# Performance work log

Measured on AMD Instinct MI355X. Metric: run time of the kernel, lower is better.

The kernel has to match this reference:

```python
import jax, jax.numpy as jnp
import numpy as np

B, S, D = 1, 1024, 1024
NH, DH, DR = 8, 128, 64
DCQ, DC = 768, 256
INTER, E, TOPK = 512, 8, 2

def rmsnorm(x, w, eps=1e-6):
    return x * jax.lax.rsqrt(jnp.mean(x * x, -1, keepdims=True) + eps) * w

def lin(x, w, b):
    return x @ w.T + b

def apply_rope(x, cos, sin):
    # x: [b, s, h, d]; cos/sin: [S, d//2]; complex rotate pairs (even, odd)
    b, s, h, d = x.shape
    xr = x.reshape(b, s, h, d // 2, 2)
    x0, x1 = xr[..., 0], xr[..., 1]
    c = cos[None, :s, None, :]
    sn = sin[None, :s, None, :]
    return jnp.stack([x0 * c - x1 * sn, x0 * sn + x1 * c], -1).reshape(b, s, h, d)

def setup_inputs():
    keys = iter(jax.random.split(jax.random.key(0), 64))
    def nrm(*shape):
        return jax.random.normal(next(keys), shape, jnp.float32) * 0.02
    theta = 1.0 / (10000.0 ** (jnp.arange(0, DR, 2, dtype=jnp.float32) / DR))
    ang = jnp.arange(S, dtype=jnp.float32)[:, None] * theta[None, :]
    return dict(
        h=jax.random.normal(next(keys), (B, S, D), jnp.float32),
        freqs_cos=jnp.cos(ang), freqs_sin=jnp.sin(ang),
        mask=jnp.triu(jnp.ones((S, S), bool), 1),
        attn_norm_w=jnp.ones(D), ffn_norm_w=jnp.ones(D),
        wq_down=nrm(DCQ, D), bq_down=jnp.zeros(DCQ), q_norm_w=jnp.ones(DCQ),
        wqc=nrm(NH * DH, DCQ), bqc=jnp.zeros(NH * DH),
        wqr=nrm(NH * DR, DCQ), bqr=jnp.zeros(NH * DR),
        wkr=nrm(DR, D), bkr=jnp.zeros(DR), kr_norm_w=jnp.ones(DR),
        wkv_down=nrm(DC, D), bkv_down=jnp.zeros(DC), kv_norm_w=jnp.ones(DC),
        wkc=nrm(NH * DH, DC), bkc=jnp.zeros(NH * DH),
        wvc=nrm(NH * DH, DC), bvc=jnp.zeros(NH * DH),
        wo=nrm(D, NH * DH), bo=jnp.zeros(D),
        sw1=nrm(INTER, D), sb1=jnp.zeros(INTER), sw2=nrm(D, INTER), sb2=jnp.zeros(D),
        sw3=nrm(INTER, D), sb3=jnp.zeros(INTER),
        ew1=nrm(E, INTER, D), eb1=jnp.zeros((E, INTER)), ew2=nrm(E, D, INTER), eb2=jnp.zeros((E, D)),
        ew3=nrm(E, INTER, D), eb3=jnp.zeros((E, INTER)),
        centroids=jax.random.normal(next(keys), (E, D), jnp.float32), biases=jnp.zeros(E),
    )

def _forward(h, freqs_cos, freqs_sin, mask, attn_norm_w, ffn_norm_w, wq_down, bq_down, q_norm_w, wqc, bqc, wqr, bqr, wkr, bkr, kr_norm_w, wkv_down, bkv_down, kv_norm_w, wkc, bkc, wvc, bvc, wo, bo, sw1, sb1, sw2, sb2, sw3, sb3, ew1, eb1, ew2, eb2, ew3, eb3, centroids, biases):
    b, s, _ = h.shape
    # --- pre-norm MLA attention ---
    x = rmsnorm(h, attn_norm_w)
    cQ = rmsnorm(lin(x, wq_down, bq_down), q_norm_w)
    qR = apply_rope(lin(cQ, wqr, bqr).reshape(b, s, NH, DR), freqs_cos, freqs_sin)
    qC = lin(cQ, wqc, bqc).reshape(b, s, NH, DH)
    q = jnp.concatenate([qC, qR], -1)                      # [b,s,NH,DH+DR]
    kR = apply_rope(rmsnorm(lin(x, wkr, bkr), kr_norm_w).reshape(b, s, 1, DR), freqs_cos, freqs_sin)
    cKV = rmsnorm(lin(x, wkv_down, bkv_down), kv_norm_w)
    kC = lin(cKV, wkc, bkc).reshape(b, s, NH, DH)
    vC = lin(cKV, wvc, bvc).reshape(b, s, NH, DH)
    k = jnp.concatenate([jnp.broadcast_to(kR, (b, s, NH, DR)), kC], -1)  # source order: [kR, kC]
    scores = jnp.einsum('bqhd,bkhd->bhqk', q, k) / jnp.sqrt(jnp.float32(DH + DR))
    scores = jnp.where(mask[None, None], jnp.finfo(scores.dtype).min, scores)
    attw = jax.nn.softmax(scores, -1)                      # dropout in eval mode = identity
    attn = jnp.einsum('bhqk,bkhd->bqhd', attw, vC).reshape(b, s, NH * DH)
    x1 = h + lin(attn, wo, bo)
    # --- pre-norm MoE FFN ---
    y = rmsnorm(x1, ffn_norm_w)
    shared = lin(jax.nn.silu(lin(y, sw1, sb1)) * lin(y, sw3, sb3), sw2, sb2)  # mean over 1 shared expert
    affinity = jax.nn.sigmoid(y @ centroids.T)             # [b,s,E]
    _, topi = jax.lax.top_k(affinity + biases, TOPK)
    gates = jax.nn.softmax(jnp.take_along_axis(affinity, topi, -1), -1)      # [b,s,TOPK]
    combine = (jax.nn.one_hot(topi, E, dtype=y.dtype) * gates[..., None]).sum(-2)  # [b,s,E]
    h1 = jax.nn.silu(jnp.einsum('bsd,eid->bsei', y, ew1) + eb1) * (jnp.einsum('bsd,eid->bsei', y, ew3) + eb3)
    out_e = jnp.einsum('bsei,edi->bsed', h1, ew2) + eb2
    routed = (out_e * combine[..., None]).sum(2)
    return x1 + shared + routed

def reference(h, freqs_cos, freqs_sin, mask, attn_norm_w, ffn_norm_w, wq_down, bq_down, q_norm_w, wqc, bqc, wqr, bqr, wkr, bkr, kr_norm_w, wkv_down, bkv_down, kv_norm_w, wkc, bkc, wvc, bvc, wo, bo, sw1, sb1, sw2, sb2, sw3, sb3, ew1, eb1, ew2, eb2, ew3, eb3, centroids, biases):
    return _forward(h, freqs_cos, freqs_sin, mask, attn_norm_w, ffn_norm_w, wq_down, bq_down, q_norm_w, wqc, bqc, wqr, bqr, wkr, bkr, kr_norm_w, wkv_down, bkv_down, kv_norm_w, wkc, bkc, wvc, bvc, wo, bo, sw1, sb1, sw2, sb2, sw3, sb3, ew1, eb1, ew2, eb2, ew3, eb3, centroids, biases)
```

## Files before the change

kernel.cpp:

```cpp
#include <hip/hip_runtime.h>

typedef unsigned short u16;
typedef __attribute__((ext_vector_type(8))) short short8;
typedef __attribute__((ext_vector_type(4))) float f32x4;

__device__ __forceinline__ float b2f(u16 u) { return __uint_as_float(((unsigned)u) << 16); }
__device__ __forceinline__ u16 f2b(float f) {
    unsigned x = __float_as_uint(f);
    return (u16)((x + 0x7fffu + ((x >> 16) & 1u)) >> 16);
}

#define GLDS16(gp, lp) __builtin_amdgcn_global_load_lds( \
    (const __attribute__((address_space(1))) void*)(gp), \
    (__attribute__((address_space(3))) void*)(lp), 16, 0, 0)

#define WAITV(N) do { \
    asm volatile("s_waitcnt vmcnt(" #N ")" ::: "memory"); \
    __builtin_amdgcn_sched_barrier(0); \
} while (0)

#define KC8_SWZ(lane) ((((lane) & 3) ^ (((lane) >> 3) & 3)) << 3)
#define RD_SWZ(fm, fq) (((fq) ^ (((fm) >> 1) & 3)) << 3)

struct Seg { const u16* W; const float* bias; void* C; int ldc; int epi; int bx0; int aidx; };
struct GArgs {
    const u16* A[2]; int lda[2]; int K[2];
    Seg seg[4]; int nseg;
    const float* res;
    float* dst2;
};

__launch_bounds__(256)
__global__ void mgemm4(GArgs ga)
{
    __shared__ u16 As[6 * 2048];
    __shared__ u16 Bs[6 * 2048];
    int bx = blockIdx.x, by = blockIdx.y;
    int si = 0;
#pragma unroll
    for (int i = 1; i < 4; i++)
        if (i < ga.nseg && bx >= ga.seg[i].bx0) si = i;
    const u16* Wp = ga.seg[si].W;
    const float* bp = ga.seg[si].bias;
    void* Cp = ga.seg[si].C;
    const int ldco = ga.seg[si].ldc;
    const int epi = ga.seg[si].epi;
    const int ai = ga.seg[si].aidx;
    const u16* Ap = ga.A[ai];
    const int lda = ga.lda[ai], K = ga.K[ai];
    const int col0 = (bx - ga.seg[si].bx0) * 64;
    const int row0 = by * 64;

    int tid = threadIdx.x;
    int lane = tid & 63, w = tid >> 6;
    int r0 = (w << 4) + (lane >> 2), kc8 = KC8_SWZ(lane);
    const u16* gA = Ap + (size_t)(row0 + r0) * lda + kc8;
    const u16* gB = Wp + (size_t)(col0 + r0) * lda + kc8;

    int fm = lane & 15, fq = lane >> 4;
    const int so = RD_SWZ(fm, fq);
    f32x4 acc[4] = {};

#define MG_STAGE(BS, KO) do { \
    GLDS16(gA + (KO), As + (BS) * 2048 + (w << 9)); \
    GLDS16(gB + (KO), Bs + (BS) * 2048 + (w << 9)); \
} while (0)

    const int nst = K >> 5;
    MG_STAGE(0, 0); MG_STAGE(1, 32); MG_STAGE(2, 64); MG_STAGE(3, 96);
    int bcur = 0;
    for (int t = 0; t < nst; t += 2) {
        if (t < nst - 2) { WAITV(4); } else { WAITV(0); }
        __builtin_amdgcn_s_barrier();
        int w4 = bcur + 4; if (w4 >= 6) w4 -= 6;
        int w5 = w4 + 1;   if (w5 >= 6) w5 -= 6;
        if (t + 4 < nst) MG_STAGE(w4, (t + 4) << 5);
        if (t + 5 < nst) MG_STAGE(w5, (t + 5) << 5);
#pragma unroll
        for (int sub = 0; sub < 2; sub++) {
            int bc = bcur + sub; if (bc >= 6) bc -= 6;
            short8 af = *(const short8*)(As + bc * 2048 + (w << 9) + fm * 32 + so);
            short8 bf[4];
#pragma unroll
            for (int nt = 0; nt < 4; nt++)
                bf[nt] = *(const short8*)(Bs + bc * 2048 + ((nt << 4) + fm) * 32 + so);
#pragma unroll
            for (int nt = 0; nt < 4; nt++)
                acc[nt] = __builtin_amdgcn_mfma_f32_16x16x32_bf16(af, bf[nt], acc[nt], 0, 0, 0);
        }
        bcur += 2; if (bcur >= 6) bcur -= 6;
    }
#undef MG_STAGE

    int rbase = row0 + (w << 4) + (fq << 2);
#pragma unroll
    for (int nt = 0; nt < 4; nt++) {
        int c = col0 + (nt << 4) + fm;
        float bcol = bp[c];
#pragma unroll
        for (int reg = 0; reg < 4; reg++) {
            int r = rbase + reg;
            float v = acc[nt][reg] + bcol;
            if (epi == 3)
                ((u16*)Cp)[(size_t)r * ldco + c] = f2b(v);
            else if (epi == 1) {
                float o = v + ga.res[(size_t)r * ldco + c];
                ((float*)Cp)[(size_t)r * ldco + c] = o;
                if (ga.dst2) ga.dst2[(size_t)r * ldco + c] = o;
            } else
                ((float*)Cp)[(size_t)r * ldco + c] = v;
        }
    }
}

__launch_bounds__(256)
__global__ void mega_glu(const u16* __restrict__ Y16,
                         const u16* __restrict__ sw1, const float* __restrict__ sb1,
                         const u16* __restrict__ sw3, const float* __restrict__ sb3,
                         const u16* __restrict__ ew1, const float* __restrict__ eb1,
                         const u16* __restrict__ ew3, const float* __restrict__ eb3,
                         u16* __restrict__ Gb,
                         const int* __restrict__ lists, const int* __restrict__ counts)
{
    __shared__ u16 As[6 * 2048];
    __shared__ u16 B1s[6 * 2048];
    __shared__ u16 B3s[6 * 2048];
    int bx = blockIdx.x, by = blockIdx.y, z = blockIdx.z;
    int col0 = bx * 64;
    int cnt = 1024; const int* list = nullptr;
    const u16 *W1p, *W3p; const float *b1p, *b3p;
    if (z == 0) {
        W1p = sw1; b1p = sb1; W3p = sw3; b3p = sb3;
    } else {
        int e = z - 1; cnt = counts[e]; list = lists + (e << 10);
        W1p = ew1 + (size_t)e * 512 * 1024; b1p = eb1 + e * 512;
        W3p = ew3 + (size_t)e * 512 * 1024; b3p = eb3 + e * 512;
    }
    int row0 = by * 64;
    if (row0 >= cnt) return;
    u16* Cp = Gb + (size_t)z * 524288;

    int tid = threadIdx.x, lane = tid & 63, w = tid >> 6;
    int r0 = (w << 4) + (lane >> 2), kc8 = KC8_SWZ(lane);
    int ar = row0 + r0;
    if (z > 0) ar = list[ar < cnt ? ar : cnt - 1];
    const u16* gA = Y16 + (size_t)ar * 1024 + kc8;
    const u16* gB1 = W1p + (size_t)(col0 + r0) * 1024 + kc8;
    const u16* gB3 = W3p + (size_t)(col0 + r0) * 1024 + kc8;

    int fm = lane & 15, fq = lane >> 4;
    const int so = RD_SWZ(fm, fq);
    f32x4 accU[4] = {}, accV[4] = {};

#define GL_STAGE(BS, KO) do { \
    GLDS16(gA + (KO),  As  + (BS) * 2048 + (w << 9)); \
    GLDS16(gB1 + (KO), B1s + (BS) * 2048 + (w << 9)); \
    GLDS16(gB3 + (KO), B3s + (BS) * 2048 + (w << 9)); \
} while (0)

    GL_STAGE(0, 0); GL_STAGE(1, 32); GL_STAGE(2, 64); GL_STAGE(3, 96);
    int bcur = 0;
    for (int t = 0; t < 32; t += 2) {
        if (t < 30) { WAITV(6); } else { WAITV(0); }
        __builtin_amdgcn_s_barrier();
        int w4 = bcur + 4; if (w4 >= 6) w4 -= 6;
        int w5 = w4 + 1;   if (w5 >= 6) w5 -= 6;
        if (t + 4 < 32) GL_STAGE(w4, (t + 4) << 5);
        if (t + 5 < 32) GL_STAGE(w5, (t + 5) << 5);
#pragma unroll
        for (int sub = 0; sub < 2; sub++) {
            int bc = bcur + sub; if (bc >= 6) bc -= 6;
            short8 af = *(const short8*)(As + bc * 2048 + (w << 9) + fm * 32 + so);
#pragma unroll
            for (int nt = 0; nt < 4; nt++) {
                short8 b1 = *(const short8*)(B1s + bc * 2048 + ((nt << 4) + fm) * 32 + so);
                accU[nt] = __builtin_amdgcn_mfma_f32_16x16x32_bf16(af, b1, accU[nt], 0, 0, 0);
            }
#pragma unroll
            for (int nt = 0; nt < 4; nt++) {
                short8 b3 = *(const short8*)(B3s + bc * 2048 + ((nt << 4) + fm) * 32 + so);
                accV[nt] = __builtin_amdgcn_mfma_f32_16x16x32_bf16(af, b3, accV[nt], 0, 0, 0);
            }
        }
        bcur += 2; if (bcur >= 6) bcur -= 6;
    }
#undef GL_STAGE

    int rbase = row0 + (w << 4) + (fq << 2);
#pragma unroll
    for (int nt = 0; nt < 4; nt++) {
        int c = col0 + (nt << 4) + fm;
        float b1c = b1p[c], b3c = b3p[c];
#pragma unroll
        for (int reg = 0; reg < 4; reg++) {
            int r = rbase + reg;
            if (r >= cnt) continue;
            float u = b2f(f2b(accU[nt][reg] + b1c));
            float v = b2f(f2b(accV[nt][reg] + b3c));
            Cp[(size_t)r * 512 + c] = f2b(u / (1.f + __expf(-u)) * v);
        }
    }
}

__launch_bounds__(256)
__global__ void mega_down(const u16* __restrict__ Gb,
                          const u16* __restrict__ sw2, const float* __restrict__ sb2,
                          const u16* __restrict__ ew2, const float* __restrict__ eb2,
                          float* __restrict__ out,
                          const int* __restrict__ lists, const float* __restrict__ glist,
                          const int* __restrict__ counts)
{
    __shared__ u16 Gs[6 * 2048];
    __shared__ u16 Ws[6 * 2048];
    int bx = blockIdx.x, by = blockIdx.y, z = blockIdx.z;
    int cnt = 1024; const int* list = nullptr; const float* gl = nullptr;
    const u16* Wp; const float* bp;
    if (z == 0) { Wp = sw2; bp = sb2; }
    else {
        int e = z - 1;
        cnt = counts[e]; list = lists + (e << 10); gl = glist + (e << 10);
        Wp = ew2 + (size_t)e * 1024 * 512; bp = eb2 + e * 1024;
    }
    int row0 = by * 64;
    if (row0 >= cnt) return;
    const u16* Ap = Gb + (size_t)z * 524288;
    int col0 = bx * 64;

    int tid = threadIdx.x, lane = tid & 63, w = tid >> 6;
    int r0 = (w << 4) + (lane >> 2), kc8 = KC8_SWZ(lane);
    const u16* gG = Ap + (size_t)(row0 + r0) * 512 + kc8;
    const u16* gW = Wp + (size_t)(col0 + r0) * 512 + kc8;

    int fm = lane & 15, fq = lane >> 4;
    const int so = RD_SWZ(fm, fq);
    f32x4 acc[4] = {};

#define MD_STAGE(BS, KO) do { \
    GLDS16(gG + (KO), Gs + (BS) * 2048 + (w << 9)); \
    GLDS16(gW + (KO), Ws + (BS) * 2048 + (w << 9)); \
} while (0)

    MD_STAGE(0, 0); MD_STAGE(1, 32); MD_STAGE(2, 64); MD_STAGE(3, 96);
    int bcur = 0;
    for (int t = 0; t < 16; t += 2) {
        if (t < 14) { WAITV(4); } else { WAITV(0); }
        __builtin_amdgcn_s_barrier();
        int w4 = bcur + 4; if (w4 >= 6) w4 -= 6;
        int w5 = w4 + 1;   if (w5 >= 6) w5 -= 6;
        if (t + 4 < 16) MD_STAGE(w4, (t + 4) << 5);
        if (t + 5 < 16) MD_STAGE(w5, (t + 5) << 5);
#pragma unroll
        for (int sub = 0; sub < 2; sub++) {
            int bc = bcur + sub; if (bc >= 6) bc -= 6;
            short8 af = *(const short8*)(Gs + bc * 2048 + (w << 9) + fm * 32 + so);
            short8 bf[4];
#pragma unroll
            for (int nt = 0; nt < 4; nt++)
                bf[nt] = *(const short8*)(Ws + bc * 2048 + ((nt << 4) + fm) * 32 + so);
#pragma unroll
            for (int nt = 0; nt < 4; nt++)
                acc[nt] = __builtin_amdgcn_mfma_f32_16x16x32_bf16(af, bf[nt], acc[nt], 0, 0, 0);
        }
        bcur += 2; if (bcur >= 6) bcur -= 6;
    }
#undef MD_STAGE

    int rbase = row0 + (w << 4) + (fq << 2);
#pragma unroll
    for (int nt = 0; nt < 4; nt++) {
        int c = col0 + (nt << 4) + fm;
        float bcol = bp[c];
#pragma unroll
        for (int reg = 0; reg < 4; reg++) {
            int r = rbase + reg;
            int tok; float g;
            if (z == 0) { tok = r; g = 1.f; }
            else { if (r >= cnt) continue; tok = list[r]; g = gl[r]; }
            atomicAdd(&out[(size_t)tok * 1024 + c], g * (acc[nt][reg] + bcol));
        }
    }
}

__launch_bounds__(256)
__global__ void attn_mfma(const u16* __restrict__ Qp, const u16* __restrict__ Kp,
                          const u16* __restrict__ VT,
                          float* __restrict__ Opart, float* __restrict__ MLp)
{
    const int qt = blockIdx.x, h = blockIdx.y, z = blockIdx.z;
    const int q0 = qt * 64;
    const int tid = threadIdx.x;
    const int lane = tid & 63, w = tid >> 6;
    const int fm = lane & 15, fq = lane >> 4;

    __shared__ u16 Ks[2 * 12288];
    __shared__ u16 Vs[4 * 4096];
    __shared__ u16 Ps[4 * 2048];

    const u16* qrow = Qp + ((size_t)h * 1024 + q0 + w * 16 + fm) * 192;
    short8 qf[6];
#pragma unroll
    for (int c = 0; c < 6; c++)
        qf[c] = *(const short8*)(qrow + c * 32 + fq * 8);

    const u16* Kb = Kp + (size_t)h * 1024 * 192;
    const u16* Vb = VT + (size_t)h * 128 * 1024;

    float m_i[4], l_i[4];
#pragma unroll
    for (int r = 0; r < 4; r++) { m_i[r] = -1e30f; l_i[r] = 0.f; }
    f32x4 accO[8] = {};
    const float scale = 0.07216878364870323f;
    const int nkt = (qt >> 1) + 1;
    const int half0 = (nkt + 1) >> 1;
    const int ktlo = z ? half0 : 0;
    const int kthi = z ? nkt : half0;
    const int rbase = w * 16 + fq * 4;

    for (int kt = ktlo; kt < kthi; ++kt) {
        const int kt0 = kt * 128;
#pragma unroll
        for (int half = 0; half < 2; half++) {
            const int o = kt0 + half * 64;
#pragma unroll
            for (int i = 0; i < 6; i++) {
                int idx = w + 4 * i;
                int c = idx >> 2, k4 = idx & 3;
                const u16* g = Kb + (size_t)(o + k4 * 16 + (lane >> 2)) * 192 + c * 32 + (lane & 3) * 8;
                GLDS16(g, Ks + half * 12288 + c * 2048 + k4 * 512 + lane * 8);
            }
#pragma unroll
            for (int i = 0; i < 4; i++) {
                int idx = w + 4 * i;
                int kc = idx >> 3, k8 = idx & 7;
                const u16* g = Vb + (size_t)(k8 * 16 + (lane >> 2)) * 1024 + o + kc * 32 + (lane & 3) * 8;
                GLDS16(g, Vs + (half * 2 + kc) * 4096 + k8 * 512 + lane * 8);
            }
        }
        __syncthreads();
        f32x4 sacc[8];
        __builtin_amdgcn_s_setprio(1);
#pragma unroll
        for (int nt = 0; nt < 8; nt++) {
            sacc[nt] = (f32x4){0.f, 0.f, 0.f, 0.f};
#pragma unroll
            for (int c = 0; c < 6; c++) {
                short8 kf = *(const short8*)(Ks + (nt >> 2) * 12288 + c * 2048 + ((nt & 3) * 16 + fm) * 32 + fq * 8);
                sacc[nt] = __builtin_amdgcn_mfma_f32_16x16x32_bf16(qf[c], kf, sacc[nt], 0, 0, 0);
            }
        }
        __builtin_amdgcn_s_setprio(0);
        float pv[8][4], rmax[4];
#pragma unroll
        for (int reg = 0; reg < 4; reg++) {
            int q = q0 + rbase + reg;
            float mx = -1e30f;
#pragma unroll
            for (int nt = 0; nt < 8; nt++) {
                int gk = kt0 + nt * 16 + fm;
                float s = sacc[nt][reg] * scale;
                if (gk > q) s = -1e30f;
                pv[nt][reg] = s;
                mx = fmaxf(mx, s);
            }
            rmax[reg] = mx;
        }
#pragma unroll
        for (int m = 1; m < 16; m <<= 1)
#pragma unroll
            for (int reg = 0; reg < 4; reg++)
                rmax[reg] = fmaxf(rmax[reg], __shfl_xor(rmax[reg], m));
        float alpha[4], rsum[4];
#pragma unroll
        for (int reg = 0; reg < 4; reg++) {
            float mn = fmaxf(m_i[reg], rmax[reg]);
            alpha[reg] = __expf(m_i[reg] - mn);
            m_i[reg] = mn;
            float s = 0.f;
#pragma unroll
            for (int nt = 0; nt < 8; nt++) {
                float p = __expf(pv[nt][reg] - mn);
                pv[nt][reg] = p;
                s += p;
            }
            rsum[reg] = s;
        }
#pragma unroll
        for (int m = 1; m < 16; m <<= 1)
#pragma unroll
            for (int reg = 0; reg < 4; reg++)
                rsum[reg] += __shfl_xor(rsum[reg], m);
#pragma unroll
        for (int reg = 0; reg < 4; reg++)
            l_i[reg] = l_i[reg] * alpha[reg] + rsum[reg];
#pragma unroll
        for (int nt = 0; nt < 8; nt++)
#pragma unroll
            for (int reg = 0; reg < 4; reg++)
                Ps[w * 2048 + (nt >> 1) * 512 + (fq * 4 + reg) * 32 + (nt & 1) * 16 + fm]
                    = f2b(pv[nt][reg]);
#pragma unroll
        for (int n2 = 0; n2 < 8; n2++)
#pragma unroll
            for (int reg = 0; reg < 4; reg++)
                accO[n2][reg] *= alpha[reg];
        short8 pf[4];
#pragma unroll
        for (int kc = 0; kc < 4; kc++)
            pf[kc] = *(const short8*)(Ps + w * 2048 + kc * 512 + fm * 32 + fq * 8);
        __builtin_amdgcn_s_setprio(1);
#pragma unroll
        for (int n2 = 0; n2 < 8; n2++)
#pragma unroll
            for (int kc = 0; kc < 4; kc++) {
                short8 vf = *(const short8*)(Vs + kc * 4096 + (n2 * 16 + fm) * 32 + fq * 8);
                accO[n2] = __builtin_amdgcn_mfma_f32_16x16x32_bf16(pf[kc], vf, accO[n2], 0, 0, 0);
            }
        __builtin_amdgcn_s_setprio(0);
        __syncthreads();
    }
    float* Ob = Opart + ((size_t)(z * 8 + h) * 1024) * 128;
#pragma unroll
    for (int reg = 0; reg < 4; reg++) {
        int row = q0 + rbase + reg;
#pragma unroll
        for (int n2 = 0; n2 < 8; n2++)
            Ob[(size_t)row * 128 + n2 * 16 + fm] = accO[n2][reg];
        if (fm == 0) {
            MLp[((size_t)(z * 8 + h) * 1024 + row) * 2]     = m_i[reg];
            MLp[((size_t)(z * 8 + h) * 1024 + row) * 2 + 1] = l_i[reg];
        }
    }
}

__launch_bounds__(256)
__global__ void attn_combine(const float* __restrict__ Opart,
                             const float* __restrict__ MLp,
                             u16* __restrict__ O)
{
    int tid = threadIdx.x;
    int rowg = blockIdx.x * 16 + (tid >> 4);
    int h = rowg >> 10, row = rowg & 1023;
    int c0 = (tid & 15) * 8;
    const float* O0 = Opart + ((size_t)h * 1024 + row) * 128;
    const float* O1 = Opart + ((size_t)(8 + h) * 1024 + row) * 128;
    float m0 = MLp[((size_t)h * 1024 + row) * 2];
    float l0 = MLp[((size_t)h * 1024 + row) * 2 + 1];
    float m1 = MLp[((size_t)(8 + h) * 1024 + row) * 2];
    float l1 = MLp[((size_t)(8 + h) * 1024 + row) * 2 + 1];
    float M = fmaxf(m0, m1);
    float w0 = __expf(m0 - M), w1 = __expf(m1 - M);
    float inv = 1.f / (l0 * w0 + l1 * w1);
#pragma unroll
    for (int j = 0; j < 8; j++) {
        float o = (O0[c0 + j] * w0 + O1[c0 + j] * w1) * inv;
        O[(size_t)row * 1024 + h * 128 + c0 + j] = f2b(o);
    }
}

__launch_bounds__(256)
__global__ void rmsnorm2x(const float* __restrict__ X0, const float* __restrict__ w0,
                          u16* __restrict__ O0, int c0,
                          const float* __restrict__ X1, const float* __restrict__ w1,
                          u16* __restrict__ O1, int c1)
{
    int b = blockIdx.x, tid = threadIdx.x;
    const float* X; const float* w; u16* O; int cols; int r;
    if (b < 1024) { X = X0; w = w0; O = O0; cols = c0; r = b; }
    else          { X = X1; w = w1; O = O1; cols = c1; r = b - 1024; }
    const float* xr = X + (size_t)r * cols;
    float ss = 0.f;
    for (int j = tid; j < cols; j += 256) { float v = xr[j]; ss += v * v; }
    __shared__ float red[256];
    red[tid] = ss; __syncthreads();
    for (int st = 128; st > 0; st >>= 1) { if (tid < st) red[tid] += red[tid + st]; __syncthreads(); }
    float scale = rsqrtf(red[0] / cols + 1e-6f);
    for (int j = tid; j < cols; j += 256)
        O[(size_t)r * cols + j] = f2b(xr[j] * scale * w[j]);
}

__launch_bounds__(256)
__global__ void rmsnorm_route(const float* __restrict__ X1, const float* __restrict__ ffnw,
                              u16* __restrict__ Y16,
                              const float* __restrict__ cent, const float* __restrict__ biases,
                              int* __restrict__ counts, int* __restrict__ lists,
                              float* __restrict__ glist)
{
    __shared__ float red[256];
    int b = blockIdx.x, tid = threadIdx.x;
    if (b < 1024) {
        int r = b;
        const float* xr = X1 + (size_t)r * 1024;
        float ss = 0.f;
        for (int j = tid; j < 1024; j += 256) { float v = xr[j]; ss += v * v; }
        red[tid] = ss; __syncthreads();
        for (int st = 128; st > 0; st >>= 1) { if (tid < st) red[tid] += red[tid + st]; __syncthreads(); }
        float scale = rsqrtf(red[0] / 1024.f + 1e-6f);
        for (int j = tid; j < 1024; j += 256)
            Y16[(size_t)r * 1024 + j] = f2b(xr[j] * scale * ffnw[j]);
    } else {
        int t = b - 1024;
        const float* xr = X1 + (size_t)t * 1024;
        float ss = 0.f;
        float acc[8] = {};
        for (int j = tid; j < 1024; j += 256) {
            float x = xr[j];
            ss += x * x;
            float yp = x * ffnw[j];
#pragma unroll
            for (int e = 0; e < 8; e++) acc[e] += yp * cent[e * 1024 + j];
        }
        red[tid] = ss; __syncthreads();
        for (int st = 128; st > 0; st >>= 1) { if (tid < st) red[tid] += red[tid + st]; __syncthreads(); }
        float scale = rsqrtf(red[0] / 1024.f + 1e-6f);
        __syncthreads();
        __shared__ float aff[8];
        for (int e = 0; e < 8; e++) {
            red[tid] = acc[e]; __syncthreads();
            for (int st = 128; st > 0; st >>= 1) { if (tid < st) red[tid] += red[tid + st]; __syncthreads(); }
            if (tid == 0) aff[e] = 1.f / (1.f + expf(-red[0] * scale));
            __syncthreads();
        }
        if (tid == 0) {
            float sb[8];
#pragma unroll
            for (int e = 0; e < 8; e++) sb[e] = aff[e] + biases[e];
            int i0 = 0;
            for (int e = 1; e < 8; e++) if (sb[e] > sb[i0]) i0 = e;
            int i1 = -1;
            for (int e = 0; e < 8; e++) { if (e == i0) continue; if (i1 < 0 || sb[e] > sb[i1]) i1 = e; }
            float a0 = aff[i0], a1 = aff[i1];
            float mx = fmaxf(a0, a1);
            float e0 = expf(a0 - mx), e1 = expf(a1 - mx);
            float inv = 1.f / (e0 + e1);
            int p0 = atomicAdd(&counts[i0], 1);
            lists[i0 * 1024 + p0] = t; glist[i0 * 1024 + p0] = e0 * inv;
            int p1 = atomicAdd(&counts[i1], 1);
            lists[i1 * 1024 + p1] = t; glist[i1 * 1024 + p1] = e1 * inv;
        }
    }
}

__launch_bounds__(256)
__global__ void pack_all(const float* __restrict__ QC, const float* __restrict__ QRr,
                         const float* __restrict__ KRraw, const float* __restrict__ krw,
                         const float* __restrict__ KC,
                         const u16* __restrict__ VCb,
                         const float* __restrict__ fcos, const float* __restrict__ fsin,
                         u16* __restrict__ Qp, u16* __restrict__ Kp, u16* __restrict__ VT)
{
    __shared__ u16 Ts[64][68];
    __shared__ float kshared[64];
    int b = blockIdx.x, tid = threadIdx.x;
    if (b < 1024) {
        int s = b;
        if (tid < 64) {
            float v = KRraw[(size_t)s * 64 + tid];
            float ss = v * v;
#pragma unroll
            for (int m = 1; m < 64; m <<= 1) ss += __shfl_xor(ss, m);
            float scale = rsqrtf(ss / 64.f + 1e-6f);
            int j = tid >> 1;
            float c = fcos[s * 32 + j], sn = fsin[s * 32 + j];
            float x0 = KRraw[(size_t)s * 64 + (tid & ~1)] * scale * krw[tid & ~1];
            float x1 = KRraw[(size_t)s * 64 + (tid | 1)]  * scale * krw[tid | 1];
            kshared[tid] = (tid & 1) ? (x0 * sn + x1 * c) : (x0 * c - x1 * sn);
        }
        __syncthreads();
        for (int e = tid; e < 1536; e += 256) {
            int h = e / 192, d = e % 192;
            float q;
            if (d < 128) {
                q = QC[(size_t)s * 1024 + h * 128 + d];
            } else {
                int dd = d - 128, j = dd >> 1;
                float c = fcos[s * 32 + j], sn = fsin[s * 32 + j];
                float x0 = QRr[(size_t)s * 512 + h * 64 + (dd & ~1)];
                float x1 = QRr[(size_t)s * 512 + h * 64 + (dd | 1)];
                q = (dd & 1) ? (x0 * sn + x1 * c) : (x0 * c - x1 * sn);
            }
            Qp[((size_t)h * 1024 + s) * 192 + d] = f2b(q);
            float k = (d < 64) ? kshared[d]
                               : KC[(size_t)s * 1024 + h * 128 + d - 64];
            Kp[((size_t)h * 1024 + s) * 192 + d] = f2b(k);
        }
    } else {
        int idx = b - 1024;
        int s0 = (idx & 15) * 64, d0 = (idx >> 4) * 64;
        for (int k = 0; k < 16; k++) {
            int e = tid + k * 256, r = e >> 6, c = e & 63;
            Ts[r][c] = VCb[(size_t)(s0 + r) * 1024 + d0 + c];
        }
        __syncthreads();
        for (int k = 0; k < 16; k++) {
            int e = tid + k * 256, d = e >> 6, s = e & 63;
            VT[(size_t)(d0 + d) * 1024 + s0 + s] = Ts[s][d];
        }
    }
}

#define NCAST 4096
__launch_bounds__(256)
__global__ void fused_cast(const float* p0, const float* p1, const float* p2,
                           const float* p3, const float* p4, const float* p5,
                           const float* p6, const float* p7, const float* p8,
                           const float* p9, const float* p10, const float* p11,
                           const float* p12, const float* pkr,
                           u16* __restrict__ dst,
                           const float* __restrict__ hX, const float* __restrict__ attnw,
                           u16* __restrict__ X16)
{
    __shared__ float red[256];
    int b = blockIdx.x, tid = threadIdx.x;
    if (b < NCAST) {
        const int NQ = 18022400 / 4;
        for (int i = b * 256 + tid; i < NQ; i += NCAST * 256) {
            int e = i * 4;
            const float* s; int base;
            if      (e <   786432) { s = p0;  base = 0; }
            else if (e <  1048576) { s = p1;  base =   786432; }
            else if (e <  1835008) { s = p2;  base =  1048576; }
            else if (e <  2228224) { s = p3;  base =  1835008; }
            else if (e <  2490368) { s = p4;  base =  2228224; }
            else if (e <  2752512) { s = p5;  base =  2490368; }
            else if (e <  3801088) { s = p6;  base =  2752512; }
            else if (e <  4325376) { s = p7;  base =  3801088; }
            else if (e <  4849664) { s = p8;  base =  4325376; }
            else if (e <  5373952) { s = p9;  base =  4849664; }
            else if (e <  9568256) { s = p10; base =  5373952; }
            else if (e < 13762560) { s = p11; base =  9568256; }
            else if (e < 17956864) { s = p12; base = 13762560; }
            else                   { s = pkr; base = 17956864; }
            float4 v = *(const float4*)(s + (e - base));
            ushort4 o;
            o.x = f2b(v.x); o.y = f2b(v.y); o.z = f2b(v.z); o.w = f2b(v.w);
            *(ushort4*)(dst + e) = o;
        }
    } else {
        int r = b - NCAST;
        const float* xr = hX + (size_t)r * 1024;
        float ss = 0.f;
        for (int j = tid; j < 1024; j += 256) { float v = xr[j]; ss += v * v; }
        red[tid] = ss; __syncthreads();
        for (int st = 128; st > 0; st >>= 1) { if (tid < st) red[tid] += red[tid + st]; __syncthreads(); }
        float scale = rsqrtf(red[0] / 1024.f + 1e-6f);
        for (int j = tid; j < 1024; j += 256)
            X16[(size_t)r * 1024 + j] = f2b(xr[j] * scale * attnw[j]);
    }
}

extern "C" void kernel_launch(void* const* d_in, const int* in_sizes, int n_in,
                              void* d_out, int out_size, void* d_ws, size_t ws_size,
                              hipStream_t stream)
{
    (void)in_sizes; (void)n_in; (void)ws_size; (void)out_size;
    const float* h       = (const float*)d_in[0];
    const float* fcos    = (const float*)d_in[1];
    const float* fsin    = (const float*)d_in[2];
    const float* attn_w  = (const float*)d_in[4];
    const float* ffn_w   = (const float*)d_in[5];
    const float* wq_down = (const float*)d_in[6];
    const float* bq_down = (const float*)d_in[7];
    const float* q_norm  = (const float*)d_in[8];
    const float* wqc     = (const float*)d_in[9];
    const float* bqc     = (const float*)d_in[10];
    const float* wqr     = (const float*)d_in[11];
    const float* bqr     = (const float*)d_in[12];
    const float* wkr     = (const float*)d_in[13];
    const float* bkr     = (const float*)d_in[14];
    const float* kr_norm = (const float*)d_in[15];
    const float* wkv     = (const float*)d_in[16];
    const float* bkv     = (const float*)d_in[17];
    const float* kv_norm = (const float*)d_in[18];
    const float* wkc     = (const float*)d_in[19];
    const float* bkc     = (const float*)d_in[20];
    const float* wvc     = (const float*)d_in[21];
    const float* bvc     = (const float*)d_in[22];
    const float* wo      = (const float*)d_in[23];
    const float* bo      = (const float*)d_in[24];
    const float* sw1     = (const float*)d_in[25];
    const float* sb1     = (const float*)d_in[26];
    const float* sw2     = (const float*)d_in[27];
    const float* sb2     = (const float*)d_in[28];
    const float* sw3     = (const float*)d_in[29];
    const float* sb3     = (const float*)d_in[30];
    const float* ew1     = (const float*)d_in[31];
    const float* eb1     = (const float*)d_in[32];
    const float* ew2     = (const float*)d_in[33];
    const float* eb2     = (const float*)d_in[34];
    const float* ew3     = (const float*)d_in[35];
    const float* eb3     = (const float*)d_in[36];
    const float* cent    = (const float*)d_in[37];
    const float* biases  = (const float*)d_in[38];

    char* wsb = (char*)d_ws;
    const size_t U5 = 512 * 1024;
    u16*   X16   = (u16*)(wsb + 8 * U5);
    float* QRr   = (float*)(wsb + 12 * U5);
    float* CQraw = (float*)(wsb + 16 * U5);
    u16*   ATT16 = (u16*)(wsb + 16 * U5);
    u16*   CQ16  = (u16*)(wsb + 22 * U5);
    float* CKVraw= (float*)(wsb + 25 * U5);
    u16*   CKV16 = (u16*)(wsb + 27 * U5);
    float* KRraw = (float*)(wsb + 28 * U5);
    float* QC    = (float*)(wsb + 29 * U5);
    float* KC    = (float*)(wsb + 37 * U5);
    float* X1    = (float*)(wsb + 53 * U5);
    float* GL    = (float*)(wsb + 61 * U5);
    int*   lists = (int*)(wsb + 61 * U5 + 32 * 1024);
    int*   counts= (int*)(wsb + 61 * U5 + 64 * 1024);
    u16*   Y16   = (u16*)(wsb + 69 * U5);
    u16*   Gb    = (u16*)(wsb + 73 * U5);

    u16* wb = (u16*)(wsb + 92 * U5);
    u16 *c_wq  = wb;
    u16 *c_wkv = c_wq  + 786432;
    u16 *c_wqc = c_wkv + 262144;
    u16 *c_wqr = c_wqc + 786432;
    u16 *c_wkc = c_wqr + 393216;
    u16 *c_wvc = c_wkc + 262144;
    u16 *c_wo  = c_wvc + 262144;
    u16 *c_sw1 = c_wo  + 1048576;
    u16 *c_sw3 = c_sw1 + 524288;
    u16 *c_sw2 = c_sw3 + 524288;
    u16 *c_ew1 = c_sw2 + 524288;
    u16 *c_ew3 = c_ew1 + 4194304;
    u16 *c_ew2 = c_ew3 + 4194304;
    u16 *c_wkr = c_ew2 + 4194304;
    u16* VCb = (u16*)(wsb + 92 * U5 + 36175872);
    u16* VTp = VCb + 1048576;
    u16* Qpk = VTp + 1048576;
    u16* Kpk = Qpk + 1572864;
    float* Opart = (float*)(wsb + 192 * U5);
    float* MLp   = (float*)(wsb + 209 * U5);

    fused_cast<<<NCAST + 1024, 256, 0, stream>>>(wq_down, wkv, wqc, wqr, wkc, wvc, wo,
                                                 sw1, sw3, sw2, ew1, ew3, ew2, wkr, wb,
                                                 h, attn_w, X16);

    {
        GArgs g = {};
        g.A[0] = X16; g.lda[0] = 1024; g.K[0] = 1024;
        g.seg[0] = { c_wq,  bq_down, CQraw,  768, 0, 0,  0 };
        g.seg[1] = { c_wkv, bkv,     CKVraw, 256, 0, 12, 0 };
        g.seg[2] = { c_wkr, bkr,     KRraw,  64,  0, 16, 0 };
        g.nseg = 3;
        mgemm4<<<dim3(17, 16), 256, 0, stream>>>(g);
    }
    rmsnorm2x<<<2048, 256, 0, stream>>>(CQraw, q_norm, CQ16, 768,
                                        CKVraw, kv_norm, CKV16, 256);
    {
        GArgs g = {};
        g.A[0] = CQ16;  g.lda[0] = 768; g.K[0] = 768;
        g.A[1] = CKV16; g.lda[1] = 256; g.K[1] = 256;
        g.seg[0] = { c_wqc, bqc, QC,   1024, 0, 0,  0 };
        g.seg[1] = { c_wqr, bqr, QRr,  512,  0, 16, 0 };
        g.seg[2] = { c_wkc, bkc, KC,   1024, 0, 24, 1 };
        g.seg[3] = { c_wvc, bvc, VCb,  1024, 3, 40, 1 };
        g.nseg = 4;
        mgemm4<<<dim3(56, 16), 256, 0, stream>>>(g);
    }
    pack_all<<<1280, 256, 0, stream>>>(QC, QRr, KRraw, kr_norm, KC, VCb, fcos, fsin,
                                       Qpk, Kpk, VTp);
    attn_mfma<<<dim3(16, 8, 2), 256, 0, stream>>>(Qpk, Kpk, VTp, Opart, MLp);
    attn_combine<<<512, 256, 0, stream>>>(Opart, MLp, ATT16);
    {
        GArgs g = {};
        g.A[0] = ATT16; g.lda[0] = 1024; g.K[0] = 1024;
        g.seg[0] = { c_wo, bo, X1, 1024, 1, 0, 0 };
        g.nseg = 1; g.res = h; g.dst2 = (float*)d_out;
        mgemm4<<<dim3(16, 16), 256, 0, stream>>>(g);
    }

    hipMemsetAsync(counts, 0, 32, stream);
    rmsnorm_route<<<2048, 256, 0, stream>>>(X1, ffn_w, Y16, cent, biases,
                                            counts, lists, GL);
    mega_glu<<<dim3(8, 16, 9), 256, 0, stream>>>(Y16, c_sw1, sb1, c_sw3, sb3,
                                                 c_ew1, eb1, c_ew3, eb3,
                                                 Gb, lists, counts);
    mega_down<<<dim3(16, 16, 9), 256, 0, stream>>>(Gb, c_sw2, sb2, c_ew2, eb2,
                                                   (float*)d_out, lists, GL, counts);
}
```

Measured before the change: 354.8 us.

## Swizzle blocks across XCDs, fuse attention combine, replace FFN atomics with gather combine

Adds an XCD-aware block index remap to the GEMM, GLU and down kernels so neighbouring tiles share an L2. The split-K attention combine moves into attn_mfma, where the last-finishing block of each tile, detected through an atomic flag counter, does the merge. The memset of the routing counters moves into fused_cast. The down projection now writes per-expert results to a scratch buffer instead of doing atomicAdd scatter, and a new ffn_combine kernel gathers the shared and top-2 expert outputs per token. This trades atomic contention for an extra scratch write and read pass plus one more launch.

```diff
diff --git a/kernel.cpp b/kernel.cpp
--- a/kernel.cpp
+++ b/kernel.cpp
@@ -21,6 +21,15 @@
 
 #define KC8_SWZ(lane) ((((lane) & 3) ^ (((lane) >> 3) & 3)) << 3)
 #define RD_SWZ(fm, fq) (((fq) ^ (((fm) >> 1) & 3)) << 3)
+
+__device__ __forceinline__ void xcd_swz(int& bx, int& by) {
+    if ((gridDim.x & 7) == 0 && gridDim.y == 16) {
+        int lid = bx + by * gridDim.x;
+        int q = lid >> 3, r = lid & 7;
+        by = q & 15;
+        bx = r + ((q >> 4) << 3);
+    }
+}
 
 struct Seg { const u16* W; const float* bias; void* C; int ldc; int epi; int bx0; int aidx; };
 struct GArgs {
@@ -36,6 +45,7 @@
     __shared__ u16 As[6 * 2048];
     __shared__ u16 Bs[6 * 2048];
     int bx = blockIdx.x, by = blockIdx.y;
+    xcd_swz(bx, by);
     int si = 0;
 #pragma unroll
     for (int i = 1; i < 4; i++)
@@ -126,6 +136,7 @@
     __shared__ u16 B1s[6 * 2048];
     __shared__ u16 B3s[6 * 2048];
     int bx = blockIdx.x, by = blockIdx.y, z = blockIdx.z;
+    xcd_swz(bx, by);
     int col0 = bx * 64;
     int cnt = 1024; const int* list = nullptr;
     const u16 *W1p, *W3p; const float *b1p, *b3p;
@@ -206,25 +217,26 @@
 __global__ void mega_down(const u16* __restrict__ Gb,
                           const u16* __restrict__ sw2, const float* __restrict__ sb2,
                           const u16* __restrict__ ew2, const float* __restrict__ eb2,
-                          float* __restrict__ out,
-                          const int* __restrict__ lists, const float* __restrict__ glist,
+                          float* __restrict__ Dscr,
                           const int* __restrict__ counts)
 {
     __shared__ u16 Gs[6 * 2048];
     __shared__ u16 Ws[6 * 2048];
     int bx = blockIdx.x, by = blockIdx.y, z = blockIdx.z;
-    int cnt = 1024; const int* list = nullptr; const float* gl = nullptr;
+    xcd_swz(bx, by);
+    int cnt = 1024;
     const u16* Wp; const float* bp;
     if (z == 0) { Wp = sw2; bp = sb2; }
     else {
         int e = z - 1;
-        cnt = counts[e]; list = lists + (e << 10); gl = glist + (e << 10);
+        cnt = counts[e];
         Wp = ew2 + (size_t)e * 1024 * 512; bp = eb2 + e * 1024;
     }
     int row0 = by * 64;
     if (row0 >= cnt) return;
     const u16* Ap = Gb + (size_t)z * 524288;
     int col0 = bx * 64;
+    float* Dp = Dscr + (size_t)z * 1048576;
 
     int tid = threadIdx.x, lane = tid & 63, w = tid >> 6;
     int r0 = (w << 4) + (lane >> 2), kc8 = KC8_SWZ(lane);
@@ -273,18 +285,38 @@
 #pragma unroll
         for (int reg = 0; reg < 4; reg++) {
             int r = rbase + reg;
-            int tok; float g;
-            if (z == 0) { tok = r; g = 1.f; }
-            else { if (r >= cnt) continue; tok = list[r]; g = gl[r]; }
-            atomicAdd(&out[(size_t)tok * 1024 + c], g * (acc[nt][reg] + bcol));
-        }
-    }
+            Dp[(size_t)r * 1024 + c] = acc[nt][reg] + bcol;
+        }
+    }
+}
+
+__launch_bounds__(256)
+__global__ void ffn_combine(const float* __restrict__ Dscr,
+                            const int* __restrict__ sE, const int* __restrict__ sP,
+                            const float* __restrict__ sG,
+                            float* __restrict__ out)
+{
+    int t = blockIdx.x, tid = threadIdx.x;
+    int e0 = sE[t * 2], e1 = sE[t * 2 + 1];
+    int p0 = sP[t * 2], p1 = sP[t * 2 + 1];
+    float g0 = sG[t * 2], g1 = sG[t * 2 + 1];
+    const float4* Ds = (const float4*)(Dscr + (size_t)t * 1024);
+    const float4* D0 = (const float4*)(Dscr + (size_t)(e0 + 1) * 1048576 + (size_t)p0 * 1024);
+    const float4* D1 = (const float4*)(Dscr + (size_t)(e1 + 1) * 1048576 + (size_t)p1 * 1024);
+    float4* o = (float4*)(out + (size_t)t * 1024);
+    float4 a = o[tid], s = Ds[tid], x0 = D0[tid], x1 = D1[tid];
+    a.x += s.x + g0 * x0.x + g1 * x1.x;
+    a.y += s.y + g0 * x0.y + g1 * x1.y;
+    a.z += s.z + g0 * x0.z + g1 * x1.z;
+    a.w += s.w + g0 * x0.w + g1 * x1.w;
+    o[tid] = a;
 }
 
 __launch_bounds__(256)
 __global__ void attn_mfma(const u16* __restrict__ Qp, const u16* __restrict__ Kp,
                           const u16* __restrict__ VT,
-                          float* __restrict__ Opart, float* __restrict__ MLp)
+                          float* __restrict__ Opart, float* __restrict__ MLp,
+                          int* __restrict__ flags, u16* __restrict__ O16)
 {
     const int qt = blockIdx.x, h = blockIdx.y, z = blockIdx.z;
     const int q0 = qt * 64;
@@ -430,30 +462,34 @@
             MLp[((size_t)(z * 8 + h) * 1024 + row) * 2 + 1] = l_i[reg];
         }
     }
-}
-
-__launch_bounds__(256)
-__global__ void attn_combine(const float* __restrict__ Opart,
-                             const float* __restrict__ MLp,
-                             u16* __restrict__ O)
-{
-    int tid = threadIdx.x;
-    int rowg = blockIdx.x * 16 + (tid >> 4);
-    int h = rowg >> 10, row = rowg & 1023;
-    int c0 = (tid & 15) * 8;
-    const float* O0 = Opart + ((size_t)h * 1024 + row) * 128;
-    const float* O1 = Opart + ((size_t)(8 + h) * 1024 + row) * 128;
-    float m0 = MLp[((size_t)h * 1024 + row) * 2];
-    float l0 = MLp[((size_t)h * 1024 + row) * 2 + 1];
-    float m1 = MLp[((size_t)(8 + h) * 1024 + row) * 2];
-    float l1 = MLp[((size_t)(8 + h) * 1024 + row) * 2 + 1];
-    float M = fmaxf(m0, m1);
-    float w0 = __expf(m0 - M), w1 = __expf(m1 - M);
-    float inv = 1.f / (l0 * w0 + l1 * w1);
-#pragma unroll
-    for (int j = 0; j < 8; j++) {
-        float o = (O0[c0 + j] * w0 + O1[c0 + j] * w1) * inv;
-        O[(size_t)row * 1024 + h * 128 + c0 + j] = f2b(o);
+    __shared__ int oldv_s;
+    __threadfence();
+    __syncthreads();
+    if (tid == 0)
+        oldv_s = __hip_atomic_fetch_add(flags + qt * 8 + h, 1,
+                                        __ATOMIC_ACQ_REL, __HIP_MEMORY_SCOPE_AGENT);
+    __syncthreads();
+    if (oldv_s != 1) return;
+    __threadfence();
+    const float* O0 = Opart + ((size_t)h * 1024) * 128;
+    const float* O1 = Opart + ((size_t)(8 + h) * 1024) * 128;
+    for (int i = tid; i < 2048; i += 256) {
+        int row = q0 + (i >> 5);
+        int c4 = (i & 31) << 2;
+        float m0 = MLp[((size_t)h * 1024 + row) * 2];
+        float l0 = MLp[((size_t)h * 1024 + row) * 2 + 1];
+        float m1 = MLp[((size_t)(8 + h) * 1024 + row) * 2];
+        float l1 = MLp[((size_t)(8 + h) * 1024 + row) * 2 + 1];
+        float M = fmaxf(m0, m1);
+        float w0 = __expf(m0 - M), w1 = __expf(m1 - M);
+        float inv = 1.f / (l0 * w0 + l1 * w1);
+        float4 a = *(const float4*)(O0 + (size_t)row * 128 + c4);
+        float4 b = *(const float4*)(O1 + (size_t)row * 128 + c4);
+        u16* op = O16 + (size_t)row * 1024 + h * 128 + c4;
+        op[0] = f2b((a.x * w0 + b.x * w1) * inv);
+        op[1] = f2b((a.y * w0 + b.y * w1) * inv);
+        op[2] = f2b((a.z * w0 + b.z * w1) * inv);
+        op[3] = f2b((a.w * w0 + b.w * w1) * inv);
     }
 }
 
@@ -483,7 +519,8 @@
                               u16* __restrict__ Y16,
                               const float* __restrict__ cent, const float* __restrict__ biases,
                               int* __restrict__ counts, int* __restrict__ lists,
-                              float* __restrict__ glist)
+                              int* __restrict__ sE, int* __restrict__ sP,
+                              float* __restrict__ sG)
 {
     __shared__ float red[256];
     int b = blockIdx.x, tid = threadIdx.x;
@@ -533,9 +570,11 @@
             float e0 = expf(a0 - mx), e1 = expf(a1 - mx);
             float inv = 1.f / (e0 + e1);
             int p0 = atomicAdd(&counts[i0], 1);
-            lists[i0 * 1024 + p0] = t; glist[i0 * 1024 + p0] = e0 * inv;
+            lists[i0 * 1024 + p0] = t;
             int p1 = atomicAdd(&counts[i1], 1);
-            lists[i1 * 1024 + p1] = t; glist[i1 * 1024 + p1] = e1 * inv;
+            lists[i1 * 1024 + p1] = t;
+            sE[t * 2] = i0; sP[t * 2] = p0; sG[t * 2] = e0 * inv;
+            sE[t * 2 + 1] = i1; sP[t * 2 + 1] = p1; sG[t * 2 + 1] = e1 * inv;
         }
     }
 }
@@ -607,7 +646,7 @@
                            const float* p12, const float* pkr,
                            u16* __restrict__ dst,
                            const float* __restrict__ hX, const float* __restrict__ attnw,
-                           u16* __restrict__ X16)
+                           u16* __restrict__ X16, int* __restrict__ zc)
 {
     __shared__ float red[256];
     int b = blockIdx.x, tid = threadIdx.x;
@@ -637,6 +676,7 @@
         }
     } else {
         int r = b - NCAST;
+        if (r == 0 && tid < 136) zc[tid] = 0;
         const float* xr = hX + (size_t)r * 1024;
         float ss = 0.f;
         for (int j = tid; j < 1024; j += 256) { float v = xr[j]; ss += v * v; }
@@ -705,9 +745,12 @@
     float* QC    = (float*)(wsb + 29 * U5);
     float* KC    = (float*)(wsb + 37 * U5);
     float* X1    = (float*)(wsb + 53 * U5);
-    float* GL    = (float*)(wsb + 61 * U5);
+    int*   counts= (int*)(wsb + 61 * U5 + 64 * 1024);
+    int*   flags = counts + 8;
     int*   lists = (int*)(wsb + 61 * U5 + 32 * 1024);
-    int*   counts= (int*)(wsb + 61 * U5 + 64 * 1024);
+    int*   sE    = (int*)(wsb + 61 * U5 + 72 * 1024);
+    int*   sP    = (int*)(wsb + 61 * U5 + 80 * 1024);
+    float* sG    = (float*)(wsb + 61 * U5 + 88 * 1024);
     u16*   Y16   = (u16*)(wsb + 69 * U5);
     u16*   Gb    = (u16*)(wsb + 73 * U5);
 
@@ -732,10 +775,11 @@
     u16* Kpk = Qpk + 1572864;
     float* Opart = (float*)(wsb + 192 * U5);
     float* MLp   = (float*)(wsb + 209 * U5);
+    float* Dscr  = (float*)(wsb + 224 * U5);
 
     fused_cast<<<NCAST + 1024, 256, 0, stream>>>(wq_down, wkv, wqc, wqr, wkc, wvc, wo,
                                                  sw1, sw3, sw2, ew1, ew3, ew2, wkr, wb,
-                                                 h, attn_w, X16);
+                                                 h, attn_w, X16, counts);
 
     {
         GArgs g = {};
@@ -761,8 +805,8 @@
     }
     pack_all<<<1280, 256, 0, stream>>>(QC, QRr, KRraw, kr_norm, KC, VCb, fcos, fsin,
                                        Qpk, Kpk, VTp);
-    attn_mfma<<<dim3(16, 8, 2), 256, 0, stream>>>(Qpk, Kpk, VTp, Opart, MLp);
-    attn_combine<<<512, 256, 0, stream>>>(Opart, MLp, ATT16);
+    attn_mfma<<<dim3(16, 8, 2), 256, 0, stream>>>(Qpk, Kpk, VTp, Opart, MLp,
+                                                  flags, ATT16);
     {
         GArgs g = {};
         g.A[0] = ATT16; g.lda[0] = 1024; g.K[0] = 1024;
@@ -771,12 +815,12 @@
         mgemm4<<<dim3(16, 16), 256, 0, stream>>>(g);
     }
 
-    hipMemsetAsync(counts, 0, 32, stream);
     rmsnorm_route<<<2048, 256, 0, stream>>>(X1, ffn_w, Y16, cent, biases,
-                                            counts, lists, GL);
+                                            counts, lists, sE, sP, sG);
     mega_glu<<<dim3(8, 16, 9), 256, 0, stream>>>(Y16, c_sw1, sb1, c_sw3, sb3,
                                                  c_ew1, eb1, c_ew3, eb3,
                                                  Gb, lists, counts);
     mega_down<<<dim3(16, 16, 9), 256, 0, stream>>>(Gb, c_sw2, sb2, c_ew2, eb2,
-                                                   (float*)d_out, lists, GL, counts);
-}
+                                                   Dscr, counts);
+    ffn_combine<<<1024, 256, 0, stream>>>(Dscr, sE, sP, sG, (float*)d_out);
+}
```

Result: slower. 387.6 us (+9.2%).
